# Kernel tuning notes

Hardware: AMD Instinct MI355X
Metric: run time of the kernel (lower is better)

Reference implementation:

```python
import jax, jax.numpy as jnp
import numpy as np

N_NODES = 50000
N_EDGES = 800000
IN_DIM = 256
FPH = 32
HEADS = 8
HIDDEN = FPH * HEADS  # 256
NUM_CLASSES = 40
NEG_SLOPE = 0.2


def gat_conv(x, W, a_src, a_dst, b, src, dst):
    """PyG GATConv (add_self_loops=False, concat heads).
    x: [N, Fin], W: [Fin, H*F], a_src/a_dst: [H, F], b: [H*F]."""
    H, F = a_src.shape
    h = (x @ W).reshape(-1, H, F)                       # [N, H, F]
    alpha_s = jnp.einsum('nhf,hf->nh', h, a_src)        # [N, H]
    alpha_d = jnp.einsum('nhf,hf->nh', h, a_dst)        # [N, H]
    e = jax.nn.leaky_relu(alpha_s[src] + alpha_d[dst], NEG_SLOPE)  # [E, H]
    # segment softmax over incoming edges of each dst node
    m = jax.ops.segment_max(e, dst, num_segments=N_NODES)          # [N, H]
    ex = jnp.exp(e - m[dst])                                        # [E, H]
    s = jax.ops.segment_sum(ex, dst, num_segments=N_NODES)          # [N, H]
    alpha = ex / (s[dst] + 1e-16)                                   # [E, H]
    msg = h[src] * alpha[:, :, None]                                # [E, H, F]
    out = jax.ops.segment_sum(msg, dst, num_segments=N_NODES)       # [N, H, F]
    return out.reshape(-1, H * F) + b


def setup_inputs() -> dict:
    key = jax.random.key(0)
    ks = jax.random.split(key, 12)
    x = jax.random.normal(ks[0], (N_NODES, IN_DIM), dtype=jnp.float32)
    edge_index = jax.random.randint(ks[1], (2, N_EDGES), 0, N_NODES, dtype=jnp.int32)
    g = lambda k, shp, fan: jax.random.normal(k, shp, dtype=jnp.float32) * np.sqrt(2.0 / fan).astype(np.float32)
    # layer 1: in=256 -> heads=8, fph=32 (concat -> 256)
    W1 = g(ks[2], (IN_DIM, HIDDEN), IN_DIM)
    a_src1 = g(ks[3], (HEADS, FPH), FPH)
    a_dst1 = g(ks[4], (HEADS, FPH), FPH)
    b1 = jnp.zeros((HIDDEN,), dtype=jnp.float32)
    # layer 2: 256 -> num_classes, heads=1
    W2 = g(ks[5], (HIDDEN, NUM_CLASSES), HIDDEN)
    a_src2 = g(ks[6], (1, NUM_CLASSES), NUM_CLASSES)
    a_dst2 = g(ks[7], (1, NUM_CLASSES), NUM_CLASSES)
    b2 = jnp.zeros((NUM_CLASSES,), dtype=jnp.float32)
    return {"x": x, "edge_index": edge_index, "W1": W1, "a_src1": a_src1,
            "a_dst1": a_dst1, "b1": b1, "W2": W2, "a_src2": a_src2,
            "a_dst2": a_dst2, "b2": b2}


def reference(x, edge_index, W1, a_src1, a_dst1, b1, W2, a_src2, a_dst2, b2):
    src, dst = edge_index[0], edge_index[1]
    h = gat_conv(x, W1, a_src1, a_dst1, b1, src, dst)
    h = jax.nn.elu(h)
    out = gat_conv(h, W2, a_src2, a_dst2, b2, src, dst)
    return out
```

## Files before the change

### kernel.cpp

```cpp
#include <hip/hip_runtime.h>
#include <hip/hip_bf16.h>
#include <math.h>

#define IN_DIM 256
#define HIDDEN 256
#define HEADS 8
#define FPH 32
#define NCLS 40

typedef __attribute__((ext_vector_type(8))) short bf16x8;
typedef __attribute__((ext_vector_type(4))) float f32x4;

__device__ inline unsigned short f2bf(float f) {
    unsigned int u = __float_as_uint(f);
    unsigned int r = (u + 0x7FFF + ((u >> 16) & 1)) >> 16;
    return (unsigned short)r;
}
__device__ inline float bf2f(unsigned short u) {
    return __uint_as_float(((unsigned int)u) << 16);
}

__global__ void hist_kernel(const int* __restrict__ dst, int* __restrict__ deg,
                            int* __restrict__ rank, int E) {
    int e = blockIdx.x * blockDim.x + threadIdx.x;
    if (e < E) rank[e] = atomicAdd(&deg[dst[e]], 1);
}

__global__ __launch_bounds__(1024) void scan_blocks_kernel(const int* __restrict__ deg,
                                                           int* __restrict__ excl,
                                                           int* __restrict__ bsum, int N) {
    __shared__ int sm[1024];
    int t = threadIdx.x;
    int g = blockIdx.x * 1024 + t;
    int v = (g < N) ? deg[g] : 0;
    sm[t] = v;
    __syncthreads();
    for (int o = 1; o < 1024; o <<= 1) {
        int add = (t >= o) ? sm[t - o] : 0;
        __syncthreads();
        sm[t] += add;
        __syncthreads();
    }
    if (g < N) excl[g] = sm[t] - v;
    if (t == 1023) bsum[blockIdx.x] = sm[1023];
}

__global__ void add_base_kernel(const int* __restrict__ excl, const int* __restrict__ bsum,
                                int* __restrict__ offs, int N, int nb) {
    int g = blockIdx.x * blockDim.x + threadIdx.x;
    if (g > N) return;
    int nblk = g >> 10;
    int lim = (g == N) ? nb : nblk;
    int base = 0;
    for (int i = 0; i < lim; i++) base += bsum[i];
    if (g < N) {
        offs[g] = excl[g] + base;
    } else {
        offs[N] = base;
    }
}

__global__ void fill_kernel(const int* __restrict__ src, const int* __restrict__ dst,
                            const int* __restrict__ rank, const int* __restrict__ offs,
                            int* __restrict__ adjsrc, int E) {
    int e = blockIdx.x * blockDim.x + threadIdx.x;
    if (e < E) {
        int d = dst[e];
        adjsrc[offs[d] + rank[e]] = src[e];
    }
}

__global__ void prep_kernel(const float* __restrict__ W1, const float* __restrict__ W2,
                            const float* __restrict__ a_src1, const float* __restrict__ a_dst1,
                            const float* __restrict__ a_src2, const float* __restrict__ a_dst2,
                            unsigned short* __restrict__ W1tb, unsigned short* __restrict__ W2tb,
                            unsigned short* __restrict__ Aw) {
    int bid = blockIdx.x;
    int tid = threadIdx.x;
    if (bid < 256) {
        int k = bid, j = tid;
        float w = W1[(size_t)k * 256 + j];
        W1tb[(size_t)j * 256 + k] = f2bf(w);
        float s = w * a_src1[j];
        float d = w * a_dst1[j];
#pragma unroll
        for (int m = 1; m < 32; m <<= 1) {
            s += __shfl_xor(s, m, 64);
            d += __shfl_xor(d, m, 64);
        }
        if ((j & 31) == 0) {
            int hd = j >> 5;
            Aw[(size_t)(2 * hd) * 256 + k]     = f2bf(s);
            Aw[(size_t)(2 * hd + 1) * 256 + k] = f2bf(d);
        }
    } else {
        int c = bid - 256;
        if (c < NCLS) {
            W2tb[(size_t)c * 256 + tid] = f2bf(W2[(size_t)tid * NCLS + c]);
        } else if (c == 48 || c == 49) {
            const float* aptr = (c == 48) ? a_src2 : a_dst2;
            const float* wr = &W2[(size_t)tid * NCLS];
            float s = 0.f;
#pragma unroll
            for (int f = 0; f < NCLS; f++) s += wr[f] * aptr[f];
            W2tb[(size_t)c * 256 + tid] = f2bf(s);
        } else {
            W2tb[(size_t)c * 256 + tid] = 0;
        }
    }
}

__global__ __launch_bounds__(256) void gemm1_mfma(const float* __restrict__ A,
                                                  const unsigned short* __restrict__ Btb,
                                                  const unsigned short* __restrict__ Aw,
                                                  unsigned short* __restrict__ Cb,
                                                  float* __restrict__ as_o,
                                                  float* __restrict__ ad_o, int M) {
    __shared__ unsigned short smem[64 * 264];
    unsigned short* As = smem;
    unsigned short* Bs = smem + 64 * 40;
    unsigned short* Bsa = smem + 64 * 40 + 256 * 40;
    int t = threadIdx.x;
    int wave = t >> 6, lane = t & 63;
    int rowBase = blockIdx.x * 64;
    int lrow = lane & 15, lk = (lane >> 4) * 8;
    f32x4 acc[16] = {};
    f32x4 acca = {};
    int arow = t >> 2, akq = (t & 3) * 8;
    for (int k0 = 0; k0 < 256; k0 += 32) {
        int grow = rowBase + arow;
        float4 a0 = {0.f, 0.f, 0.f, 0.f}, a1 = {0.f, 0.f, 0.f, 0.f};
        if (grow < M) {
            a0 = *reinterpret_cast<const float4*>(&A[(size_t)grow * 256 + k0 + akq]);
            a1 = *reinterpret_cast<const float4*>(&A[(size_t)grow * 256 + k0 + akq + 4]);
        }
        ushort4 p0 = {f2bf(a0.x), f2bf(a0.y), f2bf(a0.z), f2bf(a0.w)};
        ushort4 p1 = {f2bf(a1.x), f2bf(a1.y), f2bf(a1.z), f2bf(a1.w)};
        *reinterpret_cast<ushort4*>(&As[arow * 40 + akq]) = p0;
        *reinterpret_cast<ushort4*>(&As[arow * 40 + akq + 4]) = p1;
#pragma unroll
        for (int q = 0; q < 4; q++) {
            uint4 bv = *reinterpret_cast<const uint4*>(&Btb[(size_t)t * 256 + k0 + q * 8]);
            *reinterpret_cast<uint4*>(&Bs[t * 40 + q * 8]) = bv;
        }
        if (t < 16) {
#pragma unroll
            for (int q = 0; q < 4; q++) {
                uint4 av = *reinterpret_cast<const uint4*>(&Aw[(size_t)t * 256 + k0 + q * 8]);
                *reinterpret_cast<uint4*>(&Bsa[t * 40 + q * 8]) = av;
            }
        }
        __syncthreads();
        bf16x8 a = *reinterpret_cast<const bf16x8*>(&As[(wave * 16 + lrow) * 40 + lk]);
#pragma unroll
        for (int j = 0; j < 16; j++) {
            bf16x8 b = *reinterpret_cast<const bf16x8*>(&Bs[(j * 16 + lrow) * 40 + lk]);
            acc[j] = __builtin_amdgcn_mfma_f32_16x16x32_bf16(a, b, acc[j], 0, 0, 0);
        }
        bf16x8 ba = *reinterpret_cast<const bf16x8*>(&Bsa[lrow * 40 + lk]);
        acca = __builtin_amdgcn_mfma_f32_16x16x32_bf16(a, ba, acca, 0, 0, 0);
        __syncthreads();
    }
    int r0 = (lane >> 4) * 4;
    {
        int c = lrow, hd = c >> 1;
        float* dsts = (c & 1) ? ad_o : as_o;
#pragma unroll
        for (int r = 0; r < 4; r++) {
            int row = rowBase + wave * 16 + r0 + r;
            if (row < M) dsts[row * HEADS + hd] = acca[r];
        }
    }
    __syncthreads();
    unsigned short* Co = smem;
#pragma unroll
    for (int j = 0; j < 16; j++)
#pragma unroll
        for (int r = 0; r < 4; r++)
            Co[(wave * 16 + r0 + r) * 264 + j * 16 + lrow] = f2bf(acc[j][r]);
    __syncthreads();
    int wrow = t >> 2, wchunk = (t & 3) * 64;
    int growW = rowBase + wrow;
    if (growW < M) {
#pragma unroll
        for (int q = 0; q < 8; q++) {
            uint4 v = *reinterpret_cast<const uint4*>(&Co[wrow * 264 + wchunk + q * 8]);
            *reinterpret_cast<uint4*>(&Cb[(size_t)growW * 256 + wchunk + q * 8]) = v;
        }
    }
}

__global__ __launch_bounds__(256) void gemm2_mfma(const unsigned short* __restrict__ Ab,
                                                  const unsigned short* __restrict__ Btb,
                                                  unsigned short* __restrict__ Cb,
                                                  float* __restrict__ as_o,
                                                  float* __restrict__ ad_o, int M) {
    __shared__ unsigned short As[64 * 40];
    __shared__ unsigned short Bs[64 * 40];
    int t = threadIdx.x;
    int wave = t >> 6, lane = t & 63;
    int rowBase = blockIdx.x * 64;
    int lrow = lane & 15, lk = (lane >> 4) * 8;
    f32x4 acc[4] = {};
    int srow = t >> 2, skq = (t & 3) * 8;
    for (int k0 = 0; k0 < 256; k0 += 32) {
        uint4 av = {0, 0, 0, 0};
        int grow = rowBase + srow;
        if (grow < M) av = *reinterpret_cast<const uint4*>(&Ab[(size_t)grow * 256 + k0 + skq]);
        *reinterpret_cast<uint4*>(&As[srow * 40 + skq]) = av;
        uint4 bv = *reinterpret_cast<const uint4*>(&Btb[(size_t)srow * 256 + k0 + skq]);
        *reinterpret_cast<uint4*>(&Bs[srow * 40 + skq]) = bv;
        __syncthreads();
        bf16x8 a = *reinterpret_cast<const bf16x8*>(&As[(wave * 16 + lrow) * 40 + lk]);
#pragma unroll
        for (int j = 0; j < 4; j++) {
            bf16x8 b = *reinterpret_cast<const bf16x8*>(&Bs[(j * 16 + lrow) * 40 + lk]);
            acc[j] = __builtin_amdgcn_mfma_f32_16x16x32_bf16(a, b, acc[j], 0, 0, 0);
        }
        __syncthreads();
    }
    int crow0 = rowBase + wave * 16 + (lane >> 4) * 4;
    int ccol = lane & 15;
#pragma unroll
    for (int j = 0; j < 3; j++)
#pragma unroll
        for (int r = 0; r < 4; r++) {
            int row = crow0 + r;
            if (row < M) Cb[(size_t)row * 48 + j * 16 + ccol] = f2bf(acc[j][r]);
        }
    if (ccol < 2) {
        float* dsts = ccol ? ad_o : as_o;
#pragma unroll
        for (int r = 0; r < 4; r++) {
            int row = crow0 + r;
            if (row < M) dsts[row] = acc[3][r];
        }
    }
}

__global__ __launch_bounds__(256) void agg1_kernel(const unsigned short* __restrict__ h1b,
                                                   const float* __restrict__ as,
                                                   const float* __restrict__ ad,
                                                   const int* __restrict__ offs,
                                                   const int* __restrict__ adjsrc,
                                                   const float* __restrict__ b,
                                                   unsigned short* __restrict__ outb, int N) {
    int wid = (blockIdx.x * blockDim.x + threadIdx.x) >> 6;
    int lane = threadIdx.x & 63;
    if (wid >= N) return;
    int n = wid;
    int hd = lane >> 3;
    int beg = offs[n], end = offs[n + 1];
    float adh = ad[n * HEADS + hd];
    float ssum = 0.f;
    float4 acc = {0.f, 0.f, 0.f, 0.f};
    int i = beg;
    for (; i + 8 <= end; i += 8) {
        int sidx[8];
        float av[8];
        ushort4 hv[8];
#pragma unroll
        for (int u = 0; u < 8; u++) sidx[u] = adjsrc[i + u];
#pragma unroll
        for (int u = 0; u < 8; u++) av[u] = as[sidx[u] * HEADS + hd];
#pragma unroll
        for (int u = 0; u < 8; u++)
            hv[u] = *reinterpret_cast<const ushort4*>(&h1b[(size_t)sidx[u] * HIDDEN + lane * 4]);
#pragma unroll
        for (int u = 0; u < 8; u++) {
            float e = av[u] + adh;
            e = e > 0.f ? e : 0.2f * e;
            float ex = __expf(e);
            ssum += ex;
            acc.x += ex * bf2f(hv[u].x);
            acc.y += ex * bf2f(hv[u].y);
            acc.z += ex * bf2f(hv[u].z);
            acc.w += ex * bf2f(hv[u].w);
        }
    }
    for (; i + 4 <= end; i += 4) {
        int sidx[4];
        float av[4];
        ushort4 hv[4];
#pragma unroll
        for (int u = 0; u < 4; u++) sidx[u] = adjsrc[i + u];
#pragma unroll
        for (int u = 0; u < 4; u++) av[u] = as[sidx[u] * HEADS + hd];
#pragma unroll
        for (int u = 0; u < 4; u++)
            hv[u] = *reinterpret_cast<const ushort4*>(&h1b[(size_t)sidx[u] * HIDDEN + lane * 4]);
#pragma unroll
        for (int u = 0; u < 4; u++) {
            float e = av[u] + adh;
            e = e > 0.f ? e : 0.2f * e;
            float ex = __expf(e);
            ssum += ex;
            acc.x += ex * bf2f(hv[u].x);
            acc.y += ex * bf2f(hv[u].y);
            acc.z += ex * bf2f(hv[u].z);
            acc.w += ex * bf2f(hv[u].w);
        }
    }
    for (; i < end; i++) {
        int s = adjsrc[i];
        float e = as[s * HEADS + hd] + adh;
        e = e > 0.f ? e : 0.2f * e;
        float ex = __expf(e);
        ssum += ex;
        ushort4 hv = *reinterpret_cast<const ushort4*>(&h1b[(size_t)s * HIDDEN + lane * 4]);
        acc.x += ex * bf2f(hv.x);
        acc.y += ex * bf2f(hv.y);
        acc.z += ex * bf2f(hv.z);
        acc.w += ex * bf2f(hv.w);
    }
    float inv = 1.f / (ssum + 1e-16f);
    int col = lane * 4;
    float4 o;
    o.x = acc.x * inv + b[col + 0];
    o.y = acc.y * inv + b[col + 1];
    o.z = acc.z * inv + b[col + 2];
    o.w = acc.w * inv + b[col + 3];
    o.x = o.x > 0.f ? o.x : expm1f(o.x);
    o.y = o.y > 0.f ? o.y : expm1f(o.y);
    o.z = o.z > 0.f ? o.z : expm1f(o.z);
    o.w = o.w > 0.f ? o.w : expm1f(o.w);
    ushort4 ob;
    ob.x = f2bf(o.x); ob.y = f2bf(o.y); ob.z = f2bf(o.z); ob.w = f2bf(o.w);
    *reinterpret_cast<ushort4*>(&outb[(size_t)n * HIDDEN + col]) = ob;
}

__global__ __launch_bounds__(256) void agg2_kernel(const unsigned short* __restrict__ h2b,
                                                   const float* __restrict__ as,
                                                   const float* __restrict__ ad,
                                                   const int* __restrict__ offs,
                                                   const int* __restrict__ adjsrc,
                                                   const float* __restrict__ b,
                                                   float* __restrict__ out, int N) {
    int wid = (blockIdx.x * blockDim.x + threadIdx.x) >> 6;
    int lane = threadIdx.x & 63;
    if (wid >= N) return;
    int n = wid;
    int half = lane >> 5;
    int l = lane & 31;
    bool act = l < 20;
    int beg = offs[n], end = offs[n + 1];
    float adh = ad[n];
    float ssum = 0.f;
    float acc0 = 0.f, acc1 = 0.f;
    int i = beg;
    for (; i + 8 <= end; i += 8) {
        int sidx[4];
        float av[4];
        unsigned int hv[4];
#pragma unroll
        for (int u = 0; u < 4; u++) sidx[u] = adjsrc[i + 2 * u + half];
#pragma unroll
        for (int u = 0; u < 4; u++) av[u] = as[sidx[u]];
#pragma unroll
        for (int u = 0; u < 4; u++)
            hv[u] = act ? *reinterpret_cast<const unsigned int*>(&h2b[(size_t)sidx[u] * 48 + l * 2]) : 0u;
#pragma unroll
        for (int u = 0; u < 4; u++) {
            float e = av[u] + adh;
            e = e > 0.f ? e : 0.2f * e;
            float ex = __expf(e);
            ssum += ex;
            acc0 += ex * __uint_as_float(hv[u] << 16);
            acc1 += ex * __uint_as_float(hv[u] & 0xffff0000u);
        }
    }
    for (; i < end; i += 2) {
        int idx = i + half;
        if (idx < end) {
            int s = adjsrc[idx];
            float e = as[s] + adh;
            e = e > 0.f ? e : 0.2f * e;
            float ex = __expf(e);
            ssum += ex;
            unsigned int hv = act ? *reinterpret_cast<const unsigned int*>(&h2b[(size_t)s * 48 + l * 2]) : 0u;
            acc0 += ex * __uint_as_float(hv << 16);
            acc1 += ex * __uint_as_float(hv & 0xffff0000u);
        }
    }
    acc0 += __shfl_xor(acc0, 32, 64);
    acc1 += __shfl_xor(acc1, 32, 64);
    ssum += __shfl_xor(ssum, 32, 64);
    if (half == 0 && act) {
        float inv = 1.f / (ssum + 1e-16f);
        float2 o;
        o.x = acc0 * inv + b[2 * l];
        o.y = acc1 * inv + b[2 * l + 1];
        *reinterpret_cast<float2*>(&out[(size_t)n * NCLS + 2 * l]) = o;
    }
}

extern "C" void kernel_launch(void* const* d_in, const int* in_sizes, int n_in,
                              void* d_out, int out_size, void* d_ws, size_t ws_size,
                              hipStream_t stream) {
    const float* x      = (const float*)d_in[0];
    const int*   ei     = (const int*)d_in[1];
    const float* W1     = (const float*)d_in[2];
    const float* a_src1 = (const float*)d_in[3];
    const float* a_dst1 = (const float*)d_in[4];
    const float* b1     = (const float*)d_in[5];
    const float* W2     = (const float*)d_in[6];
    const float* a_src2 = (const float*)d_in[7];
    const float* a_dst2 = (const float*)d_in[8];
    const float* b2     = (const float*)d_in[9];
    float* out = (float*)d_out;

    const int N = in_sizes[0] / IN_DIM;
    const int E = in_sizes[1] / 2;
    const int* src = ei;
    const int* dst = ei + E;

    char* ws = (char*)d_ws;
    size_t off = 0;
    auto alloc = [&](size_t bytes) {
        void* p = ws + off;
        off = (off + bytes + 255) & ~(size_t)255;
        return p;
    };
    int*   deg    = (int*)alloc((size_t)N * 4);
    int*   excl   = (int*)alloc((size_t)N * 4);
    int*   bsum   = (int*)alloc((size_t)256 * 4);
    int*   rank   = (int*)alloc((size_t)E * 4);
    int*   offs   = (int*)alloc((size_t)(N + 1) * 4);
    int*   adjsrc = (int*)alloc((size_t)E * 4);
    unsigned short* W1tb  = (unsigned short*)alloc((size_t)256 * 256 * 2);
    unsigned short* W2tb  = (unsigned short*)alloc((size_t)64 * 256 * 2);
    unsigned short* Aw    = (unsigned short*)alloc((size_t)16 * 256 * 2);
    unsigned short* h1b   = (unsigned short*)alloc((size_t)N * HIDDEN * 2);
    unsigned short* out1b = (unsigned short*)alloc((size_t)N * HIDDEN * 2);
    unsigned short* h2b   = (unsigned short*)alloc((size_t)N * 48 * 2);
    float* as1    = (float*)alloc((size_t)N * HEADS * 4);
    float* ad1    = (float*)alloc((size_t)N * HEADS * 4);
    float* as2    = (float*)alloc((size_t)N * 4);
    float* ad2    = (float*)alloc((size_t)N * 4);

    const int nb = (N + 1023) / 1024;
    const int ng1 = (N + 63) / 64;

    hipMemsetAsync(deg, 0, (size_t)N * 4, stream);
    hist_kernel<<<dim3((E + 255) / 256), dim3(256), 0, stream>>>(dst, deg, rank, E);
    scan_blocks_kernel<<<dim3(nb), dim3(1024), 0, stream>>>(deg, excl, bsum, N);
    add_base_kernel<<<dim3((N + 256) / 256), dim3(256), 0, stream>>>(excl, bsum, offs, N, nb);
    fill_kernel<<<dim3((E + 255) / 256), dim3(256), 0, stream>>>(src, dst, rank, offs, adjsrc, E);

    prep_kernel<<<dim3(320), dim3(256), 0, stream>>>(W1, W2, a_src1, a_dst1, a_src2, a_dst2,
                                                     W1tb, W2tb, Aw);

    gemm1_mfma<<<dim3(ng1), dim3(256), 0, stream>>>(x, W1tb, Aw, h1b, as1, ad1, N);
    agg1_kernel<<<dim3((N + 3) / 4), dim3(256), 0, stream>>>(h1b, as1, ad1, offs, adjsrc, b1, out1b, N);

    gemm2_mfma<<<dim3(ng1), dim3(256), 0, stream>>>(out1b, W2tb, h2b, as2, ad2, N);
    agg2_kernel<<<dim3((N + 3) / 4), dim3(256), 0, stream>>>(h2b, as2, ad2, offs, adjsrc, b2, out, N);
}
```

Measured before the change: 209.4 us.

## Merge weight prep into histogram kernel and enlarge gemm1 tile to 128 rows

The weight preprocessing kernel is folded into the edge histogram launch as extra blocks, which removes one kernel launch. gemm1 now uses 512 threads and 128-row tiles, so each block reuses the staged B tile across twice as many rows of x. The bf16 output is written back through shared memory in two halves to fit the existing LDS buffer. Risks are lower occupancy from the larger blocks and a tail block at the end of the grid.

Result: faster. 203.9 us (-2.6%).

```diff
diff --git a/kernel.cpp b/kernel.cpp
--- a/kernel.cpp
+++ b/kernel.cpp
@@ -20,10 +20,52 @@
     return __uint_as_float(((unsigned int)u) << 16);
 }
 
-__global__ void hist_kernel(const int* __restrict__ dst, int* __restrict__ deg,
-                            int* __restrict__ rank, int E) {
-    int e = blockIdx.x * blockDim.x + threadIdx.x;
-    if (e < E) rank[e] = atomicAdd(&deg[dst[e]], 1);
+__global__ void histprep_kernel(const int* __restrict__ dst, int* __restrict__ deg,
+                                int* __restrict__ rank, int E,
+                                const float* __restrict__ W1, const float* __restrict__ W2,
+                                const float* __restrict__ a_src1, const float* __restrict__ a_dst1,
+                                const float* __restrict__ a_src2, const float* __restrict__ a_dst2,
+                                unsigned short* __restrict__ W1tb, unsigned short* __restrict__ W2tb,
+                                unsigned short* __restrict__ Aw, int nhist) {
+    int bid = blockIdx.x;
+    int tid = threadIdx.x;
+    if (bid < nhist) {
+        int e = bid * 256 + tid;
+        if (e < E) rank[e] = atomicAdd(&deg[dst[e]], 1);
+        return;
+    }
+    int pbid = bid - nhist;
+    if (pbid < 256) {
+        int k = pbid, j = tid;
+        float w = W1[(size_t)k * 256 + j];
+        W1tb[(size_t)j * 256 + k] = f2bf(w);
+        float s = w * a_src1[j];
+        float d = w * a_dst1[j];
+#pragma unroll
+        for (int m = 1; m < 32; m <<= 1) {
+            s += __shfl_xor(s, m, 64);
+            d += __shfl_xor(d, m, 64);
+        }
+        if ((j & 31) == 0) {
+            int hd = j >> 5;
+            Aw[(size_t)(2 * hd) * 256 + k]     = f2bf(s);
+            Aw[(size_t)(2 * hd + 1) * 256 + k] = f2bf(d);
+        }
+    } else {
+        int c = pbid - 256;
+        if (c < NCLS) {
+            W2tb[(size_t)c * 256 + tid] = f2bf(W2[(size_t)tid * NCLS + c]);
+        } else if (c == 48 || c == 49) {
+            const float* aptr = (c == 48) ? a_src2 : a_dst2;
+            const float* wr = &W2[(size_t)tid * NCLS];
+            float s = 0.f;
+#pragma unroll
+            for (int f = 0; f < NCLS; f++) s += wr[f] * aptr[f];
+            W2tb[(size_t)c * 256 + tid] = f2bf(s);
+        } else {
+            W2tb[(size_t)c * 256 + tid] = 0;
+        }
+    }
 }
 
 __global__ __launch_bounds__(1024) void scan_blocks_kernel(const int* __restrict__ deg,
@@ -70,63 +112,24 @@
     }
 }
 
-__global__ void prep_kernel(const float* __restrict__ W1, const float* __restrict__ W2,
-                            const float* __restrict__ a_src1, const float* __restrict__ a_dst1,
-                            const float* __restrict__ a_src2, const float* __restrict__ a_dst2,
-                            unsigned short* __restrict__ W1tb, unsigned short* __restrict__ W2tb,
-                            unsigned short* __restrict__ Aw) {
-    int bid = blockIdx.x;
-    int tid = threadIdx.x;
-    if (bid < 256) {
-        int k = bid, j = tid;
-        float w = W1[(size_t)k * 256 + j];
-        W1tb[(size_t)j * 256 + k] = f2bf(w);
-        float s = w * a_src1[j];
-        float d = w * a_dst1[j];
-#pragma unroll
-        for (int m = 1; m < 32; m <<= 1) {
-            s += __shfl_xor(s, m, 64);
-            d += __shfl_xor(d, m, 64);
-        }
-        if ((j & 31) == 0) {
-            int hd = j >> 5;
-            Aw[(size_t)(2 * hd) * 256 + k]     = f2bf(s);
-            Aw[(size_t)(2 * hd + 1) * 256 + k] = f2bf(d);
-        }
-    } else {
-        int c = bid - 256;
-        if (c < NCLS) {
-            W2tb[(size_t)c * 256 + tid] = f2bf(W2[(size_t)tid * NCLS + c]);
-        } else if (c == 48 || c == 49) {
-            const float* aptr = (c == 48) ? a_src2 : a_dst2;
-            const float* wr = &W2[(size_t)tid * NCLS];
-            float s = 0.f;
-#pragma unroll
-            for (int f = 0; f < NCLS; f++) s += wr[f] * aptr[f];
-            W2tb[(size_t)c * 256 + tid] = f2bf(s);
-        } else {
-            W2tb[(size_t)c * 256 + tid] = 0;
-        }
-    }
-}
-
-__global__ __launch_bounds__(256) void gemm1_mfma(const float* __restrict__ A,
+__global__ __launch_bounds__(512) void gemm1_mfma(const float* __restrict__ A,
                                                   const unsigned short* __restrict__ Btb,
                                                   const unsigned short* __restrict__ Aw,
                                                   unsigned short* __restrict__ Cb,
                                                   float* __restrict__ as_o,
                                                   float* __restrict__ ad_o, int M) {
-    __shared__ unsigned short smem[64 * 264];
+    __shared__ unsigned short smem[16896];
     unsigned short* As = smem;
-    unsigned short* Bs = smem + 64 * 40;
-    unsigned short* Bsa = smem + 64 * 40 + 256 * 40;
+    unsigned short* Bs = smem + 128 * 40;
+    unsigned short* Bsa = smem + 128 * 40 + 256 * 40;
     int t = threadIdx.x;
     int wave = t >> 6, lane = t & 63;
-    int rowBase = blockIdx.x * 64;
+    int rowBase = blockIdx.x * 128;
     int lrow = lane & 15, lk = (lane >> 4) * 8;
     f32x4 acc[16] = {};
     f32x4 acca = {};
     int arow = t >> 2, akq = (t & 3) * 8;
+    int bcol = t >> 1, bh = (t & 1) * 16;
     for (int k0 = 0; k0 < 256; k0 += 32) {
         int grow = rowBase + arow;
         float4 a0 = {0.f, 0.f, 0.f, 0.f}, a1 = {0.f, 0.f, 0.f, 0.f};
@@ -138,10 +141,11 @@
         ushort4 p1 = {f2bf(a1.x), f2bf(a1.y), f2bf(a1.z), f2bf(a1.w)};
         *reinterpret_cast<ushort4*>(&As[arow * 40 + akq]) = p0;
         *reinterpret_cast<ushort4*>(&As[arow * 40 + akq + 4]) = p1;
-#pragma unroll
-        for (int q = 0; q < 4; q++) {
-            uint4 bv = *reinterpret_cast<const uint4*>(&Btb[(size_t)t * 256 + k0 + q * 8]);
-            *reinterpret_cast<uint4*>(&Bs[t * 40 + q * 8]) = bv;
+        {
+            uint4 bv0 = *reinterpret_cast<const uint4*>(&Btb[(size_t)bcol * 256 + k0 + bh]);
+            uint4 bv1 = *reinterpret_cast<const uint4*>(&Btb[(size_t)bcol * 256 + k0 + bh + 8]);
+            *reinterpret_cast<uint4*>(&Bs[bcol * 40 + bh]) = bv0;
+            *reinterpret_cast<uint4*>(&Bs[bcol * 40 + bh + 8]) = bv1;
         }
         if (t < 16) {
 #pragma unroll
@@ -171,21 +175,27 @@
             if (row < M) dsts[row * HEADS + hd] = acca[r];
         }
     }
-    __syncthreads();
     unsigned short* Co = smem;
 #pragma unroll
-    for (int j = 0; j < 16; j++)
-#pragma unroll
-        for (int r = 0; r < 4; r++)
-            Co[(wave * 16 + r0 + r) * 264 + j * 16 + lrow] = f2bf(acc[j][r]);
-    __syncthreads();
-    int wrow = t >> 2, wchunk = (t & 3) * 64;
-    int growW = rowBase + wrow;
-    if (growW < M) {
-#pragma unroll
-        for (int q = 0; q < 8; q++) {
-            uint4 v = *reinterpret_cast<const uint4*>(&Co[wrow * 264 + wchunk + q * 8]);
-            *reinterpret_cast<uint4*>(&Cb[(size_t)growW * 256 + wchunk + q * 8]) = v;
+    for (int h = 0; h < 2; h++) {
+        __syncthreads();
+        if ((wave >> 2) == h) {
+            int lw = wave & 3;
+#pragma unroll
+            for (int j = 0; j < 16; j++)
+#pragma unroll
+                for (int r = 0; r < 4; r++)
+                    Co[(lw * 16 + r0 + r) * 264 + j * 16 + lrow] = f2bf(acc[j][r]);
+        }
+        __syncthreads();
+        int wrow = t >> 3, wchunk = (t & 7) * 32;
+        int row = rowBase + h * 64 + wrow;
+        if (row < M) {
+#pragma unroll
+            for (int q = 0; q < 4; q++) {
+                uint4 v = *reinterpret_cast<const uint4*>(&Co[wrow * 264 + wchunk + q * 8]);
+                *reinterpret_cast<uint4*>(&Cb[(size_t)row * 256 + wchunk + q * 8]) = v;
+            }
         }
     }
 }
@@ -439,20 +449,19 @@
     float* ad2    = (float*)alloc((size_t)N * 4);
 
     const int nb = (N + 1023) / 1024;
-    const int ng1 = (N + 63) / 64;
+    const int nhist = (E + 255) / 256;
 
     hipMemsetAsync(deg, 0, (size_t)N * 4, stream);
-    hist_kernel<<<dim3((E + 255) / 256), dim3(256), 0, stream>>>(dst, deg, rank, E);
+    histprep_kernel<<<dim3(nhist + 320), dim3(256), 0, stream>>>(dst, deg, rank, E,
+                                                                 W1, W2, a_src1, a_dst1, a_src2, a_dst2,
+                                                                 W1tb, W2tb, Aw, nhist);
     scan_blocks_kernel<<<dim3(nb), dim3(1024), 0, stream>>>(deg, excl, bsum, N);
     add_base_kernel<<<dim3((N + 256) / 256), dim3(256), 0, stream>>>(excl, bsum, offs, N, nb);
     fill_kernel<<<dim3((E + 255) / 256), dim3(256), 0, stream>>>(src, dst, rank, offs, adjsrc, E);
 
-    prep_kernel<<<dim3(320), dim3(256), 0, stream>>>(W1, W2, a_src1, a_dst1, a_src2, a_dst2,
-                                                     W1tb, W2tb, Aw);
-
-    gemm1_mfma<<<dim3(ng1), dim3(256), 0, stream>>>(x, W1tb, Aw, h1b, as1, ad1, N);
+    gemm1_mfma<<<dim3((N + 127) / 128), dim3(512), 0, stream>>>(x, W1tb, Aw, h1b, as1, ad1, N);
     agg1_kernel<<<dim3((N + 3) / 4), dim3(256), 0, stream>>>(h1b, as1, ad1, offs, adjsrc, b1, out1b, N);
 
-    gemm2_mfma<<<dim3(ng1), dim3(256), 0, stream>>>(out1b, W2tb, h2b, as2, ad2, N);
+    gemm2_mfma<<<dim3((N + 63) / 64), dim3(256), 0, stream>>>(out1b, W2tb, h2b, as2, ad2, N);
     agg2_kernel<<<dim3((N + 3) / 4), dim3(256), 0, stream>>>(h2b, as2, ad2, offs, adjsrc, b2, out, N);
 }
```
